# Kernel tuning notes

Measured on AMD Instinct MI355X. Metric: run time of the kernel, lower is better.

The kernel has to match this reference:

```python
import jax, jax.numpy as jnp
import numpy as np

H, F, L, T = 256, 128, 4, 1
NG, NC, EC, EG = 8192, 65536, 524288, 32768
NCONF, NMOL = 4096, 512
CUTOFF, NGAUSS = 10.0, 50
_OFF = jnp.linspace(0.0, CUTOFF, NGAUSS)
_COEFF = -0.5 / (_OFF[1] - _OFF[0]) ** 2


def _bn(h, g, b):
    # training-mode BatchNorm1d (biased variance, eps=1e-5)
    m = h.mean(0)
    v = h.var(0)
    return (h - m) * jax.lax.rsqrt(v + 1e-5) * g + b


def setup_inputs() -> dict:
    ks = iter(jax.random.split(jax.random.key(0), 64))
    nrm = lambda sh, s=0.05: jax.random.normal(next(ks), sh, jnp.float32) * s
    inp = dict(
        pos=jax.random.normal(next(ks), (NC, 3), jnp.float32) * 3.0,
        atom_emb=nrm((9, 64, H)),
        vn_emb=jnp.zeros((H,), jnp.float32),
        cf_lin1=nrm((L, H, F)),
        cf_mlp_w1=nrm((L, NGAUSS, F)), cf_mlp_b1=jnp.zeros((L, F)),
        cf_mlp_w2=nrm((L, F, F)), cf_mlp_b2=jnp.zeros((L, F)),
        cf_lin2=nrm((L, F, H)), cf_lin2_b=jnp.zeros((L, H)),
        lin_w=nrm((L, H, H)), lin_b=jnp.zeros((L, H)),
        bond_emb=nrm((L, 3, 8, H)), gin_eps=jnp.zeros((L,)),
        gin_w1=nrm((L, H, H)), gin_b1=jnp.zeros((L, H)),
        gin_g1=jnp.ones((L, H)), gin_be1=jnp.zeros((L, H)),
        gin_w2=nrm((L, H, H)), gin_b2=jnp.zeros((L, H)),
        bn_g=jnp.ones((L, H)), bn_b=jnp.zeros((L, H)),
        vn_w1=nrm((H, H)), vn_b1=jnp.zeros((H,)),
        vn_w2=nrm((H, H)), vn_b2=jnp.zeros((H,)),
        out_w1=nrm((H, H)), out_b1=jnp.zeros((H,)),
        out_w2=nrm((H, T)), out_b2=jnp.zeros((T,)),
    )
    inp['x_atom'] = jax.random.randint(next(ks), (NG, 9), 0, 64)
    g = np.arange(NG)
    reps = NC // NG  # 8 conformers per molecule
    inp['conf_node_batch'] = jnp.asarray(np.tile(g, reps))  # conformer node -> graph node
    mol = g // (NG // NMOL)  # 16 atoms per molecule
    inp['pos_batch'] = jnp.asarray(np.concatenate([mol * reps + r for r in range(reps)]))  # -> conformer id
    inp['conf_batch'] = jnp.asarray(np.arange(NCONF) // reps)  # conformer -> molecule
    inp['edge_index_conf'] = jax.random.randint(next(ks), (2, EC), 0, NC)
    inp['edge_index_graph'] = jax.random.randint(next(ks), (2, EG), 0, NG)
    inp['edge_attr_graph'] = jax.random.randint(next(ks), (EG, 3), 0, 8)
    return inp


def _forward(pos, atom_emb, vn_emb, cf_lin1, cf_mlp_w1, cf_mlp_b1, cf_mlp_w2, cf_mlp_b2,
             cf_lin2, cf_lin2_b, lin_w, lin_b, bond_emb, gin_eps, gin_w1, gin_b1,
             gin_g1, gin_be1, gin_w2, gin_b2, bn_g, bn_b, vn_w1, vn_b1, vn_w2, vn_b2,
             out_w1, out_b1, out_w2, out_b2,
             x_atom, conf_node_batch, pos_batch, conf_batch,
             edge_index_conf, edge_index_graph, edge_attr_graph):
    relu = jax.nn.relu
    # AtomEncoder: sum of per-feature embeddings [NG,H], broadcast to conformer nodes
    xg = atom_emb[jnp.arange(9), x_atom].sum(1)
    x = xg[conf_node_batch]                                 # [NC,H]
    # radius-graph geometry (edge list precomputed)
    src, dst = edge_index_conf[0], edge_index_conf[1]
    d = jnp.linalg.norm(pos[src] - pos[dst], axis=-1)       # [EC]
    gauss = jnp.exp(_COEFF * (d[:, None] - _OFF) ** 2)      # GaussianSmearing [EC,50]
    ccut = 0.5 * (jnp.cos(d * (jnp.pi / CUTOFF)) + 1.0)     # cosine cutoff
    gsrc, gdst = edge_index_graph[0], edge_index_graph[1]
    vn = jnp.broadcast_to(vn_emb, (NCONF, H))
    for i in range(L):
        x = x + vn[pos_batch]
        if i < L - 1:
            tmp = jax.ops.segment_sum(x, pos_batch, NCONF) + vn
            vn = relu(relu(tmp @ vn_w1 + vn_b1) @ vn_w2 + vn_b2)
        out = x  # residual
        # CFConv over conformer radius graph
        We = (relu(gauss @ cf_mlp_w1[i] + cf_mlp_b1[i]) @ cf_mlp_w2[i] + cf_mlp_b2[i]) * ccut[:, None]
        h = x @ cf_lin1[i]                                  # lin1 (no bias)
        h = jax.ops.segment_sum(h[src] * We, dst, NC)
        h = relu(h @ cf_lin2[i] + cf_lin2_b[i])
        out = out + h @ lin_w[i] + lin_b[i]
        # GIN over molecular graph on conf-max-pooled nodes
        xa = jax.ops.segment_max(x, conf_node_batch, NG)
        e = bond_emb[i][jnp.arange(3), edge_attr_graph].sum(1)   # BondEncoder [EG,H]
        agg = jax.ops.segment_sum(relu(xa[gsrc] + e), gdst, NG)
        z = ((1.0 + gin_eps[i]) * xa + agg) @ gin_w1[i] + gin_b1[i]
        z = relu(_bn(z, gin_g1[i], gin_be1[i])) @ gin_w2[i] + gin_b2[i]
        z = _bn(z, bn_g[i], bn_b[i])
        out = out + z[conf_node_batch]
        x = relu(out)
    xc = jax.ops.segment_max(x, pos_batch, NCONF)
    xm = jax.ops.segment_max(xc, conf_batch, NMOL)
    return relu(xm @ out_w1 + out_b1) @ out_w2 + out_b2      # [NMOL,T]


reference = _forward
```

## Files before the change

### kernel.cpp

```cpp
#include <hip/hip_runtime.h>
#include <math.h>

#define H 256
#define F 128
#define NLAYERS 4
#define NG 8192
#define NC 65536
#define EC 524288
#define EG 32768
#define NCONF 4096
#define NMOL 512
#define NGAUSS 50
#define NTAB 8192
#define TABSTEP 0.001953125f
#define INVSTEP 512.0f

using s16x8 = __attribute__((ext_vector_type(8))) short;
using f32x4 = __attribute__((ext_vector_type(4))) float;

static __device__ __forceinline__ unsigned short f2bf(float f) {
    unsigned int u = __float_as_uint(f);
    u += 0x7fffu + ((u >> 16) & 1u);
    return (unsigned short)(u >> 16);
}
static __device__ __forceinline__ float bf2f(unsigned short b) {
    return __uint_as_float(((unsigned int)b) << 16);
}
static __device__ __forceinline__ float bflo(unsigned int u) {
    return __uint_as_float(u << 16);
}
static __device__ __forceinline__ float bfhi(unsigned int u) {
    return __uint_as_float(u & 0xffff0000u);
}


__global__ __launch_bounds__(256) void k_init_x(const float* __restrict__ atom_emb,
    const int* __restrict__ x_atom, unsigned short* __restrict__ x)
{
    int i = blockIdx.x, h = threadIdx.x;
    int g = i & (NG - 1);
    float s = 0.f;
#pragma unroll
    for (int f = 0; f < 9; ++f) {
        int a = x_atom[g * 9 + f];
        s += atom_emb[(f * 64 + a) * H + h];
    }
    x[(size_t)i * H + h] = f2bf(s);
}

__global__ __launch_bounds__(256) void k_vninit(const float* __restrict__ vn_emb,
                                                float* __restrict__ vn)
{
    vn[(size_t)blockIdx.x * H + threadIdx.x] = vn_emb[threadIdx.x];
}

template <bool DOTMP>
__global__ __launch_bounds__(256) void k_pre(unsigned short* __restrict__ X,
    const float* __restrict__ vn, float* __restrict__ tmp,
    unsigned short* __restrict__ xa)
{
    int m = blockIdx.x, h = threadIdx.x;
    float xam[16];
#pragma unroll
    for (int t = 0; t < 16; ++t) xam[t] = -3.4e38f;
#pragma unroll 2
    for (int r = 0; r < 8; ++r) {
        float vv = vn[(size_t)(m * 8 + r) * H + h];
        float ts = vv;
        size_t base = ((size_t)r * NG + m * 16) * H + h;
#pragma unroll
        for (int t = 0; t < 16; ++t) {
            float v = bf2f(X[base + (size_t)t * H]) + vv;
            X[base + (size_t)t * H] = f2bf(v);
            xam[t] = fmaxf(xam[t], v);
            ts += v;
        }
        if (DOTMP) tmp[(size_t)(m * 8 + r) * H + h] = ts;
    }
#pragma unroll
    for (int t = 0; t < 16; ++t)
        xa[(size_t)(m * 16 + t) * H + h] = f2bf(xam[t]);
}

__global__ __launch_bounds__(256) void k_bnprep(const float* __restrict__ stats,
    const float* __restrict__ gamma, const float* __restrict__ beta,
    float* __restrict__ scale, float* __restrict__ shift)
{
    int n = threadIdx.x;
    float mean = stats[n] * (1.0f / NG);
    float var = stats[256 + n] * (1.0f / NG) - mean * mean;
    float sc = gamma[n] * rsqrtf(var + 1e-5f);
    scale[n] = sc;
    shift[n] = beta[n] - mean * sc;
}

__global__ __launch_bounds__(256) void k_molmax(const unsigned short* __restrict__ x,
                                                float* __restrict__ xm)
{
    int m = blockIdx.x, h = threadIdx.x;
    float best = -3.4e38f;
    for (int r = 0; r < 8; ++r) {
        size_t base = ((size_t)r * NG + m * 16) * H + h;
#pragma unroll 4
        for (int t = 0; t < 16; ++t) best = fmaxf(best, bf2f(x[base + (size_t)t * H]));
    }
    xm[(size_t)m * H + h] = best;
}

__global__ __launch_bounds__(256) void k_head(const float* __restrict__ y1,
    const float* __restrict__ w2, const float* __restrict__ b2,
    float* __restrict__ out)
{
    __shared__ float red[256];
    int m = blockIdx.x, h = threadIdx.x;
    red[h] = y1[(size_t)m * H + h] * w2[h];
    __syncthreads();
    for (int s = 128; s > 0; s >>= 1) {
        if (h < s) red[h] += red[h + s];
        __syncthreads();
    }
    if (h == 0) out[m] = red[0] + b2[0];
}

__global__ __launch_bounds__(256) void k_wt(const float* __restrict__ W,
    unsigned short* __restrict__ Wt, int K, int N, int Kp)
{
    int l = blockIdx.y;
    W += (size_t)l * K * N;
    Wt += (size_t)l * N * Kp;
    int n = blockIdx.x;
    for (int k = threadIdx.x; k < Kp; k += 256)
        Wt[(size_t)n * Kp + k] = (k < K) ? f2bf(W[(size_t)k * N + n]) : (unsigned short)0;
}


__global__ __launch_bounds__(256) void k_hist(const int* __restrict__ dst,
                                              int* __restrict__ cnt, int ne)
{
    int e = blockIdx.x * 256 + threadIdx.x;
    if (e < ne) atomicAdd(&cnt[dst[e]], 1);
}

__global__ __launch_bounds__(256) void k_scan1(const int* __restrict__ cnt,
    int* __restrict__ part, int* __restrict__ bsum)
{
    __shared__ int sh[256];
    int t = threadIdx.x, idx = blockIdx.x * 256 + t;
    int v = cnt[idx];
    sh[t] = v; __syncthreads();
    for (int s = 1; s < 256; s <<= 1) {
        int add = (t >= s) ? sh[t - s] : 0;
        __syncthreads();
        sh[t] += add;
        __syncthreads();
    }
    part[idx] = sh[t] - v;
    if (t == 255) bsum[blockIdx.x] = sh[255];
}

__global__ __launch_bounds__(256) void k_scan2(int* __restrict__ bsum, int nb)
{
    __shared__ int sh[256];
    int t = threadIdx.x;
    int v = (t < nb) ? bsum[t] : 0;
    sh[t] = v; __syncthreads();
    for (int s = 1; s < 256; s <<= 1) {
        int add = (t >= s) ? sh[t - s] : 0;
        __syncthreads();
        sh[t] += add;
        __syncthreads();
    }
    if (t < nb) bsum[t] = sh[t] - v;
}

__global__ __launch_bounds__(256) void k_scan3(int* __restrict__ part,
    const int* __restrict__ bsum, int* __restrict__ cursor, int nbins, int total)
{
    int idx = blockIdx.x * 256 + threadIdx.x;
    int v = part[idx] + bsum[blockIdx.x];
    part[idx] = v;
    cursor[idx] = v;
    if (idx == 0) part[nbins] = total;
}

__global__ __launch_bounds__(256) void k_cperm(const float* __restrict__ pos,
    const int* __restrict__ ei, int* __restrict__ cursor,
    int* __restrict__ psrc, float2* __restrict__ pdcc)
{
    int e = blockIdx.x * 256 + threadIdx.x;
    int s = ei[e], t = ei[EC + e];
    float dx = pos[s * 3 + 0] - pos[t * 3 + 0];
    float dy = pos[s * 3 + 1] - pos[t * 3 + 1];
    float dz = pos[s * 3 + 2] - pos[t * 3 + 2];
    float dd = sqrtf(dx * dx + dy * dy + dz * dz);
    int p = atomicAdd(&cursor[t], 1);
    psrc[p] = s;
    pdcc[p] = make_float2(dd, 0.5f * (cosf(dd * 0.314159265358979f) + 1.0f));
}

__global__ __launch_bounds__(256) void k_gperm(const int* __restrict__ ei,
    const int* __restrict__ attr, int* __restrict__ cursor,
    int* __restrict__ pgsrc, int* __restrict__ pattr)
{
    int e = blockIdx.x * 256 + threadIdx.x;
    int s = ei[e], t = ei[EG + e];
    int p = atomicAdd(&cursor[t], 1);
    pgsrc[p] = s;
    pattr[p] = attr[e * 3] | (attr[e * 3 + 1] << 4) | (attr[e * 3 + 2] << 8);
}


__global__ __launch_bounds__(256) void k_cf_agg(const unsigned short* __restrict__ tab,
    const int* __restrict__ rowptr, const int* __restrict__ psrc,
    const float2* __restrict__ pdcc,
    const unsigned short* __restrict__ cfh, unsigned short* __restrict__ hagg)
{
    int slot = threadIdx.x >> 4;
    int c8 = (threadIdx.x & 15) << 3;
    int n = blockIdx.x * 16 + slot;
    int lo = rowptr[n], hi = rowptr[n + 1];
    float a[8] = {0.f, 0.f, 0.f, 0.f, 0.f, 0.f, 0.f, 0.f};
    for (int e = lo; e < hi; ++e) {
        int s = psrc[e];
        float2 dc = pdcc[e];
        float u = dc.x * INVSTEP + 0.5f;
        int it = (int)u;
        if (it > NTAB - 1) it = NTAB - 1;
        uint4 T = *(const uint4*)&tab[(size_t)it * F + c8];
        uint4 HV = *(const uint4*)&cfh[(size_t)s * F + c8];
        float cc = dc.y;
        a[0] = fmaf(bflo(T.x) * cc, bflo(HV.x), a[0]);
        a[1] = fmaf(bfhi(T.x) * cc, bfhi(HV.x), a[1]);
        a[2] = fmaf(bflo(T.y) * cc, bflo(HV.y), a[2]);
        a[3] = fmaf(bfhi(T.y) * cc, bfhi(HV.y), a[3]);
        a[4] = fmaf(bflo(T.z) * cc, bflo(HV.z), a[4]);
        a[5] = fmaf(bfhi(T.z) * cc, bfhi(HV.z), a[5]);
        a[6] = fmaf(bflo(T.w) * cc, bflo(HV.w), a[6]);
        a[7] = fmaf(bfhi(T.w) * cc, bfhi(HV.w), a[7]);
    }
    uint4 o;
    o.x = ((unsigned)f2bf(a[1]) << 16) | f2bf(a[0]);
    o.y = ((unsigned)f2bf(a[3]) << 16) | f2bf(a[2]);
    o.z = ((unsigned)f2bf(a[5]) << 16) | f2bf(a[4]);
    o.w = ((unsigned)f2bf(a[7]) << 16) | f2bf(a[6]);
    *(uint4*)&hagg[(size_t)n * F + c8] = o;
}

__global__ __launch_bounds__(256) void k_gin_agg(const unsigned short* __restrict__ xa,
    const float* __restrict__ bond, const int* __restrict__ growptr,
    const int* __restrict__ pgsrc, const int* __restrict__ pattr,
    const float* __restrict__ eps_p, unsigned short* __restrict__ agg)
{
    int g = blockIdx.x, h = threadIdx.x;
    int lo = growptr[g], hi = growptr[g + 1];
    float acc = 0.f;
    for (int e = lo; e < hi; ++e) {
        int s = pgsrc[e], a = pattr[e];
        float v = bf2f(xa[(size_t)s * H + h])
                + bond[(a & 15) * H + h]
                + bond[(8 + ((a >> 4) & 15)) * H + h]
                + bond[(16 + (a >> 8)) * H + h];
        acc += fmaxf(v, 0.f);
    }
    agg[(size_t)g * H + h] =
        f2bf((1.0f + eps_p[0]) * bf2f(xa[(size_t)g * H + h]) + acc);
}

template<int ASRC, int EPI>
__global__ __launch_bounds__(256) void mgemm(
    const float* __restrict__ Af, const unsigned short* __restrict__ Ab,
    const unsigned short* __restrict__ Bt,
    const float* __restrict__ bias,
    float* __restrict__ Cf, unsigned short* __restrict__ Cb,
    int K, int Kp, int ldc,
    const float* __restrict__ sca, const float* __restrict__ sha,
    float* __restrict__ stats_out)
{
    __shared__ unsigned short As[128][72];
    __shared__ unsigned short Bs[128][72];
    const int tid = threadIdx.x;
    const int bm = blockIdx.y * 128;
    const int bn = blockIdx.x * 128;
    const int lane = tid & 63;
    const int wid = tid >> 6;
    const int wm = wid >> 1, wn = wid & 1;
    const int rsel = lane & 15, ksel = (lane >> 4) * 8;

    f32x4 acc[4][4];
#pragma unroll
    for (int a = 0; a < 4; ++a)
#pragma unroll
        for (int b = 0; b < 4; ++b) acc[a][b] = (f32x4){0.f, 0.f, 0.f, 0.f};

    for (int k0 = 0; k0 < Kp; k0 += 64) {
#pragma unroll
        for (int i = 0; i < 4; ++i) {
            int c = tid + i * 256;
            int row = c >> 3, kc = (c & 7) * 8;
            *(uint4*)&Bs[row][kc] =
                *(const uint4*)&Bt[(size_t)(bn + row) * Kp + k0 + kc];
        }
        if constexpr (ASRC == 0 || ASRC == 4) {
#pragma unroll
            for (int i = 0; i < 8; ++i) {
                int c = tid + i * 256;
                int row = c >> 4, kc = (c & 15) * 4;
                float4 v = *(const float4*)&Af[(size_t)(bm + row) * K + k0 + kc];
                if constexpr (ASRC == 4) {
                    float4 s4 = *(const float4*)&sca[k0 + kc];
                    float4 h4 = *(const float4*)&sha[k0 + kc];
                    v.x = fmaxf(fmaf(v.x, s4.x, h4.x), 0.f);
                    v.y = fmaxf(fmaf(v.y, s4.y, h4.y), 0.f);
                    v.z = fmaxf(fmaf(v.z, s4.z, h4.z), 0.f);
                    v.w = fmaxf(fmaf(v.w, s4.w, h4.w), 0.f);
                }
                ushort4 b;
                b.x = f2bf(v.x); b.y = f2bf(v.y); b.z = f2bf(v.z); b.w = f2bf(v.w);
                *(ushort4*)&As[row][kc] = b;
            }
        } else {
#pragma unroll
            for (int i = 0; i < 4; ++i) {
                int c = tid + i * 256;
                int row = c >> 3, kc = (c & 7) * 8;
                *(uint4*)&As[row][kc] =
                    *(const uint4*)&Ab[(size_t)(bm + row) * K + k0 + kc];
            }
        }
        __syncthreads();
#pragma unroll
        for (int kk = 0; kk < 64; kk += 32) {
            s16x8 af[4], bf[4];
#pragma unroll
            for (int mi = 0; mi < 4; ++mi)
                af[mi] = *(const s16x8*)&As[wm * 64 + mi * 16 + rsel][kk + ksel];
#pragma unroll
            for (int ni = 0; ni < 4; ++ni)
                bf[ni] = *(const s16x8*)&Bs[wn * 64 + ni * 16 + rsel][kk + ksel];
#pragma unroll
            for (int mi = 0; mi < 4; ++mi)
#pragma unroll
                for (int ni = 0; ni < 4; ++ni)
                    acc[mi][ni] = __builtin_amdgcn_mfma_f32_16x16x32_bf16(
                        af[mi], bf[ni], acc[mi][ni], 0, 0, 0);
        }
        __syncthreads();
    }

    float colS[4] = {0.f, 0.f, 0.f, 0.f};
    float colQ[4] = {0.f, 0.f, 0.f, 0.f};
#pragma unroll
    for (int mi = 0; mi < 4; ++mi) {
// ... 129 lines not shown
        __syncthreads();
#pragma unroll
        for (int kk = 0; kk < 64; kk += 32) {
            s16x8 af[4], bf[4];
#pragma unroll
            for (int mi = 0; mi < 4; ++mi)
                af[mi] = *(const s16x8*)&T1s[wm * 64 + mi * 16 + rsel][k0 + kk + ksel];
#pragma unroll
            for (int ni = 0; ni < 4; ++ni)
                bf[ni] = *(const s16x8*)&Bs[wn * 64 + ni * 16 + rsel][kk + ksel];
#pragma unroll
            for (int mi = 0; mi < 4; ++mi)
#pragma unroll
                for (int ni = 0; ni < 4; ++ni)
                    acc[mi][ni] = __builtin_amdgcn_mfma_f32_16x16x32_bf16(
                        af[mi], bf[ni], acc[mi][ni], 0, 0, 0);
        }
        __syncthreads();
    }
#pragma unroll
    for (int mi = 0; mi < 4; ++mi)
#pragma unroll
        for (int r = 0; r < 4; ++r) {
            int m = bm + wm * 64 + mi * 16 + ((lane >> 4) << 2) + r;
#pragma unroll
            for (int ni = 0; ni < 4; ++ni) {
                int n = wn * 64 + ni * 16 + (lane & 15);
                tab[(size_t)m * F + n] = f2bf(acc[mi][ni][r] + b2[n]);
            }
        }
}

__global__ __launch_bounds__(512) void k_vnmlp(
    const float* __restrict__ TMP,
    const unsigned short* __restrict__ w1, const float* __restrict__ b1,
    const unsigned short* __restrict__ w2, const float* __restrict__ b2,
    float* __restrict__ VN)
{
    __shared__ unsigned short As[128][72];
    __shared__ unsigned short Bs[256][72];
    __shared__ unsigned short Ts[128][264];
    const int tid = threadIdx.x;
    const int bm = blockIdx.x * 128;
    const int lane = tid & 63, wid = tid >> 6;
    const int wm = wid >> 2, wn = wid & 3;
    const int rsel = lane & 15, ksel = (lane >> 4) * 8;

    f32x4 acc[4][4];
#pragma unroll
    for (int a = 0; a < 4; ++a)
#pragma unroll
        for (int b = 0; b < 4; ++b) acc[a][b] = (f32x4){0.f, 0.f, 0.f, 0.f};
    for (int k0 = 0; k0 < 256; k0 += 64) {
#pragma unroll
        for (int i = 0; i < 4; ++i) {
            int c = tid + i * 512;
            int row = c >> 4, kc = (c & 15) * 4;
            float4 v = *(const float4*)&TMP[(size_t)(bm + row) * 256 + k0 + kc];
            ushort4 b;
            b.x = f2bf(v.x); b.y = f2bf(v.y); b.z = f2bf(v.z); b.w = f2bf(v.w);
            *(ushort4*)&As[row][kc] = b;
        }
#pragma unroll
        for (int i = 0; i < 4; ++i) {
            int c = tid + i * 512;
            int row = c >> 3, kc = (c & 7) * 8;
            *(uint4*)&Bs[row][kc] = *(const uint4*)&w1[(size_t)row * 256 + k0 + kc];
        }
        __syncthreads();
#pragma unroll
        for (int kk = 0; kk < 64; kk += 32) {
            s16x8 af[4], bf[4];
#pragma unroll
            for (int mi = 0; mi < 4; ++mi)
                af[mi] = *(const s16x8*)&As[wm * 64 + mi * 16 + rsel][kk + ksel];
#pragma unroll
            for (int ni = 0; ni < 4; ++ni)
                bf[ni] = *(const s16x8*)&Bs[wn * 64 + ni * 16 + rsel][kk + ksel];
#pragma unroll
            for (int mi = 0; mi < 4; ++mi)
#pragma unroll
                for (int ni = 0; ni < 4; ++ni)
                    acc[mi][ni] = __builtin_amdgcn_mfma_f32_16x16x32_bf16(
                        af[mi], bf[ni], acc[mi][ni], 0, 0, 0);
        }
        __syncthreads();
    }
#pragma unroll
    for (int mi = 0; mi < 4; ++mi)
#pragma unroll
        for (int r = 0; r < 4; ++r) {
            int mrow = wm * 64 + mi * 16 + ((lane >> 4) << 2) + r;
#pragma unroll
// ... 10 lines not shown
#pragma unroll
        for (int i = 0; i < 4; ++i) {
            int c = tid + i * 512;
            int row = c >> 3, kc = (c & 7) * 8;
            *(uint4*)&Bs[row][kc] = *(const uint4*)&w2[(size_t)row * 256 + k0 + kc];
        }
        __syncthreads();
#pragma unroll
        for (int kk = 0; kk < 64; kk += 32) {
            s16x8 af[4], bf[4];
#pragma unroll
            for (int mi = 0; mi < 4; ++mi)
                af[mi] = *(const s16x8*)&Ts[wm * 64 + mi * 16 + rsel][k0 + kk + ksel];
#pragma unroll
            for (int ni = 0; ni < 4; ++ni)
                bf[ni] = *(const s16x8*)&Bs[wn * 64 + ni * 16 + rsel][kk + ksel];
#pragma unroll
            for (int mi = 0; mi < 4; ++mi)
#pragma unroll
                for (int ni = 0; ni < 4; ++ni)
                    acc[mi][ni] = __builtin_amdgcn_mfma_f32_16x16x32_bf16(
                        af[mi], bf[ni], acc[mi][ni], 0, 0, 0);
        }
        __syncthreads();
    }
#pragma unroll
    for (int mi = 0; mi < 4; ++mi)
#pragma unroll
        for (int r = 0; r < 4; ++r) {
            int m = bm + wm * 64 + mi * 16 + ((lane >> 4) << 2) + r;
#pragma unroll
            for (int ni = 0; ni < 4; ++ni) {
                int n = wn * 64 + ni * 16 + (lane & 15);
                VN[(size_t)m * 256 + n] = fmaxf(acc[mi][ni][r] + b2[n], 0.f);
            }
        }
}

__global__ __launch_bounds__(512) void k_combine(
    const unsigned short* __restrict__ HAGG,
    const unsigned short* __restrict__ lin2t, const float* __restrict__ lin2b,
    const unsigned short* __restrict__ linwt, const float* __restrict__ linb,
    const float* __restrict__ Z2,
    const float* __restrict__ scb, const float* __restrict__ shb,
    unsigned short* __restrict__ X)
{
    __shared__ unsigned short As[128][72];
    __shared__ unsigned short Bs[256][72];
    __shared__ unsigned short H2s[128][264];
    const int tid = threadIdx.x;
    const int bm = blockIdx.x * 128;
    const int lane = tid & 63;
    const int wid = tid >> 6;
    const int wm = wid >> 2, wn = wid & 3;
    const int rsel = lane & 15, ksel = (lane >> 4) * 8;

    f32x4 acc[4][4];
#pragma unroll
    for (int a = 0; a < 4; ++a)
#pragma unroll
        for (int b = 0; b < 4; ++b) acc[a][b] = (f32x4){0.f, 0.f, 0.f, 0.f};

    for (int k0 = 0; k0 < 128; k0 += 64) {
#pragma unroll
        for (int i = 0; i < 2; ++i) {
            int c = tid + i * 512;
            int row = c >> 3, kc = (c & 7) * 8;
            *(uint4*)&As[row][kc] =
                *(const uint4*)&HAGG[(size_t)(bm + row) * 128 + k0 + kc];
        }
#pragma unroll
        for (int i = 0; i < 4; ++i) {
            int c = tid + i * 512;
            int row = c >> 3, kc = (c & 7) * 8;
            *(uint4*)&Bs[row][kc] = *(const uint4*)&lin2t[(size_t)row * 128 + k0 + kc];
        }
        __syncthreads();
#pragma unroll
// ... 27 lines not shown
        }

#pragma unroll
    for (int a = 0; a < 4; ++a)
#pragma unroll
        for (int b = 0; b < 4; ++b) acc[a][b] = (f32x4){0.f, 0.f, 0.f, 0.f};
    for (int k0 = 0; k0 < 256; k0 += 64) {
#pragma unroll
        for (int i = 0; i < 4; ++i) {
            int c = tid + i * 512;
            int row = c >> 3, kc = (c & 7) * 8;
            *(uint4*)&Bs[row][kc] = *(const uint4*)&linwt[(size_t)row * 256 + k0 + kc];
        }
        __syncthreads();
#pragma unroll
        for (int kk = 0; kk < 64; kk += 32) {
            s16x8 af[4], bf[4];
#pragma unroll
            for (int mi = 0; mi < 4; ++mi)
                af[mi] = *(const s16x8*)&H2s[wm * 64 + mi * 16 + rsel][k0 + kk + ksel];
#pragma unroll
            for (int ni = 0; ni < 4; ++ni)
                bf[ni] = *(const s16x8*)&Bs[wn * 64 + ni * 16 + rsel][kk + ksel];
#pragma unroll
            for (int mi = 0; mi < 4; ++mi)
#pragma unroll
                for (int ni = 0; ni < 4; ++ni)
                    acc[mi][ni] = __builtin_amdgcn_mfma_f32_16x16x32_bf16(
                        af[mi], bf[ni], acc[mi][ni], 0, 0, 0);
        }
        __syncthreads();
    }
#pragma unroll
    for (int mi = 0; mi < 4; ++mi)
#pragma unroll
        for (int r = 0; r < 4; ++r) {
            int m = bm + wm * 64 + mi * 16 + ((lane >> 4) << 2) + r;
            const float* z2row = &Z2[(size_t)(m & (NG - 1)) * 256];
#pragma unroll
            for (int ni = 0; ni < 4; ++ni) {
                int n = wn * 64 + ni * 16 + (lane & 15);
                size_t ix = (size_t)m * 256 + n;
                float z2v = fmaf(z2row[n], scb[n], shb[n]);
                float o = bf2f(X[ix]) + acc[mi][ni][r] + linb[n] + z2v;
                X[ix] = f2bf(fmaxf(o, 0.f));
            }
        }
}

extern "C" void kernel_launch(void* const* d_in, const int* in_sizes, int n_in,
                              void* d_out, int out_size, void* d_ws, size_t ws_size,
                              hipStream_t stream)
{
    (void)in_sizes; (void)n_in; (void)out_size; (void)ws_size;
    const float* pos       = (const float*)d_in[0];
    const float* atom_emb  = (const float*)d_in[1];
    const float* vn_emb    = (const float*)d_in[2];
    const float* cf_lin1   = (const float*)d_in[3];
    const float* cf_mlp_w1 = (const float*)d_in[4];
    const float* cf_mlp_b1 = (const float*)d_in[5];
    const float* cf_mlp_w2 = (const float*)d_in[6];
    const float* cf_mlp_b2 = (const float*)d_in[7];
    const float* cf_lin2   = (const float*)d_in[8];
    const float* cf_lin2_b = (const float*)d_in[9];
    const float* lin_w     = (const float*)d_in[10];
    const float* lin_b     = (const float*)d_in[11];
    const float* bond_emb  = (const float*)d_in[12];
    const float* gin_eps   = (const float*)d_in[13];
    const float* gin_w1    = (const float*)d_in[14];
    const float* gin_b1    = (const float*)d_in[15];
    const float* gin_g1    = (const float*)d_in[16];
    const float* gin_be1   = (const float*)d_in[17];
    const float* gin_w2    = (const float*)d_in[18];
    const float* gin_b2    = (const float*)d_in[19];
    const float* bn_g      = (const float*)d_in[20];
    const float* bn_b      = (const float*)d_in[21];
    const float* vn_w1     = (const float*)d_in[22];
    const float* vn_b1     = (const float*)d_in[23];
    const float* vn_w2     = (const float*)d_in[24];
    const float* vn_b2     = (const float*)d_in[25];
    const float* out_w1    = (const float*)d_in[26];
    const float* out_b1    = (const float*)d_in[27];
    const float* out_w2    = (const float*)d_in[28];
    const float* out_b2    = (const float*)d_in[29];
    const int* x_atom      = (const int*)d_in[30];
    const int* ei_conf     = (const int*)d_in[34];
    const int* ei_graph    = (const int*)d_in[35];
    const int* attr_graph  = (const int*)d_in[36];
    float* out = (float*)d_out;
    float* ws  = (float*)d_ws;

    size_t o = 0;
    float* Z1   = ws + o; o += (size_t)NG * H;
    float* Z2   = ws + o; o += (size_t)NG * H;
    float* VN   = ws + o; o += (size_t)NCONF * H;
    float* TMP  = ws + o; o += (size_t)NCONF * H;
    float* XM   = ws + o; o += (size_t)NMOL * H;
    float* Y1   = ws + o; o += (size_t)NMOL * H;
    float* STATS= ws + o; o += 1024;
    float* SCA  = ws + o; o += 256;
    float* SHA  = ws + o; o += 256;
    float* SCB  = ws + o; o += 256;
    float* SHB  = ws + o; o += 256;
    float* PDCC = ws + o; o += (size_t)2 * EC;
    unsigned short* XB   = (unsigned short*)(ws + o); o += (size_t)NC * H / 2;
    unsigned short* XA   = (unsigned short*)(ws + o); o += (size_t)NG * H / 2;
    unsigned short* AGGB = (unsigned short*)(ws + o); o += (size_t)NG * H / 2;
    unsigned short* CFH  = (unsigned short*)(ws + o); o += (size_t)NC * F / 2;
    unsigned short* HAGG = (unsigned short*)(ws + o); o += (size_t)NC * F / 2;
    unsigned short* TAB  = (unsigned short*)(ws + o); o += (size_t)NLAYERS * NTAB * F / 2;
    int* PSRC   = (int*)(ws + o); o += EC;
    int* PGSRC  = (int*)(ws + o); o += EG;
    int* PATTR  = (int*)(ws + o); o += EG;
    int* CNT    = (int*)(ws + o); o += NC;
    int* ROWC   = (int*)(ws + o); o += NC + 64;
    int* CURC   = (int*)(ws + o); o += NC;
    int* ROWG   = (int*)(ws + o); o += NG + 64;
    int* CURG   = (int*)(ws + o); o += NG;
    int* BSUM   = (int*)(ws + o); o += 256;
    unsigned short* WT = (unsigned short*)(ws + o);
    size_t wo = 0;
    unsigned short* lin1t = WT + wo; wo += (size_t)NLAYERS * 128 * 256;
    unsigned short* w1t   = WT + wo; wo += (size_t)NLAYERS * 128 * 64;
    unsigned short* w2t   = WT + wo; wo += (size_t)NLAYERS * 128 * 128;
    unsigned short* lin2t = WT + wo; wo += (size_t)NLAYERS * 256 * 128;
    unsigned short* linwt = WT + wo; wo += (size_t)NLAYERS * 256 * 256;
    unsigned short* g1t   = WT + wo; wo += (size_t)NLAYERS * 256 * 256;
    unsigned short* g2t   = WT + wo; wo += (size_t)NLAYERS * 256 * 256;
    unsigned short* vn1t  = WT + wo; wo += 256 * 256;
    unsigned short* vn2t  = WT + wo; wo += 256 * 256;
    unsigned short* ow1t  = WT + wo; wo += 256 * 256;

    k_wt<<<dim3(128, NLAYERS), 256, 0, stream>>>(cf_lin1,   lin1t, 256, 128, 256);
    k_wt<<<dim3(128, NLAYERS), 256, 0, stream>>>(cf_mlp_w1, w1t,    50, 128,  64);
    k_wt<<<dim3(128, NLAYERS), 256, 0, stream>>>(cf_mlp_w2, w2t,   128, 128, 128);
    k_wt<<<dim3(256, NLAYERS), 256, 0, stream>>>(cf_lin2,   lin2t, 128, 256, 128);
    k_wt<<<dim3(256, NLAYERS), 256, 0, stream>>>(lin_w,     linwt, 256, 256, 256);
    k_wt<<<dim3(256, NLAYERS), 256, 0, stream>>>(gin_w1,    g1t,   256, 256, 256);
    k_wt<<<dim3(256, NLAYERS), 256, 0, stream>>>(gin_w2,    g2t,   256, 256, 256);
    k_wt<<<dim3(256, 1), 256, 0, stream>>>(vn_w1,  vn1t, 256, 256, 256);
    k_wt<<<dim3(256, 1), 256, 0, stream>>>(vn_w2,  vn2t, 256, 256, 256);
    k_wt<<<dim3(256, 1), 256, 0, stream>>>(out_w1, ow1t, 256, 256, 256);
    k_tab<<<dim3(NTAB / 128, NLAYERS), 256, 0, stream>>>(
        w1t, cf_mlp_b1, w2t, cf_mlp_b2, TAB);

    hipMemsetAsync(CNT, 0, NC * sizeof(int), stream);
    k_hist<<<EC / 256, 256, 0, stream>>>(ei_conf + EC, CNT, EC);
    k_scan1<<<NC / 256, 256, 0, stream>>>(CNT, ROWC, BSUM);
    k_scan2<<<1, 256, 0, stream>>>(BSUM, NC / 256);
    k_scan3<<<NC / 256, 256, 0, stream>>>(ROWC, BSUM, CURC, NC, EC);
    k_cperm<<<EC / 256, 256, 0, stream>>>(pos, ei_conf, CURC, PSRC, (float2*)PDCC);

    hipMemsetAsync(CNT, 0, NG * sizeof(int), stream);
    k_hist<<<EG / 256, 256, 0, stream>>>(ei_graph + EG, CNT, EG);
    k_scan1<<<NG / 256, 256, 0, stream>>>(CNT, ROWG, BSUM);
    k_scan2<<<1, 256, 0, stream>>>(BSUM, NG / 256);
    k_scan3<<<NG / 256, 256, 0, stream>>>(ROWG, BSUM, CURG, NG, EG);
    k_gperm<<<EG / 256, 256, 0, stream>>>(ei_graph, attr_graph, CURG, PGSRC, PATTR);

    k_init_x<<<NC, 256, 0, stream>>>(atom_emb, x_atom, XB);
    k_vninit<<<NCONF, 256, 0, stream>>>(vn_emb, VN);

    for (int i = 0; i < NLAYERS; ++i) {
        if (i < NLAYERS - 1) {
            k_pre<true><<<NMOL, 256, 0, stream>>>(XB, VN, TMP, XA);
            k_vnmlp<<<NCONF / 128, 512, 0, stream>>>(TMP, vn1t, vn_b1, vn2t, vn_b2, VN);
        } else {
            k_pre<false><<<NMOL, 256, 0, stream>>>(XB, VN, TMP, XA);
        }
        mgemm<2, 6><<<dim3(1, NC / 128), 256, 0, stream>>>(
            0, XB, lin1t + (size_t)i * 128 * 256, nullptr, 0, CFH,
            256, 256, 128, 0, 0, 0);
        k_cf_agg<<<NC / 16, 256, 0, stream>>>(TAB + (size_t)i * NTAB * F,
            ROWC, PSRC, (const float2*)PDCC, CFH, HAGG);
        k_gin_agg<<<NG, 256, 0, stream>>>(
            XA, bond_emb + (size_t)i * 3 * 8 * H, ROWG, PGSRC, PATTR,
            gin_eps + i, AGGB);
        hipMemsetAsync(STATS, 0, 4096, stream);
        mgemm<2, 7><<<dim3(2, NG / 128), 256, 0, stream>>>(
            0, AGGB, g1t + (size_t)i * 256 * 256, gin_b1 + i * H, Z1, 0,
            256, 256, 256, 0, 0, STATS);
        k_bnprep<<<1, 256, 0, stream>>>(STATS, gin_g1 + i * H, gin_be1 + i * H,
                                        SCA, SHA);
        mgemm<4, 7><<<dim3(2, NG / 128), 256, 0, stream>>>(
            Z1, 0, g2t + (size_t)i * 256 * 256, gin_b2 + i * H, Z2, 0,
            256, 256, 256, SCA, SHA, STATS + 512);
        k_bnprep<<<1, 256, 0, stream>>>(STATS + 512, bn_g + i * H, bn_b + i * H,
                                        SCB, SHB);
        k_combine<<<NC / 128, 512, 0, stream>>>(
            HAGG, lin2t + (size_t)i * 256 * 128, cf_lin2_b + i * H,
            linwt + (size_t)i * 256 * 256, lin_b + i * H, Z2, SCB, SHB, XB);
    }

    k_molmax<<<NMOL, 256, 0, stream>>>(XB, XM);
    mgemm<0, 1><<<dim3(2, NMOL / 128), 256, 0, stream>>>(
        XM, 0, ow1t, out_b1, Y1, 0, 256, 256, 256, 0, 0, 0);
    k_head<<<NMOL, 256, 0, stream>>>(Y1, out_w2, out_b2, out);
}
```

Baseline: 984.9 us.

## Fold virtual-node add into consumers and fuse setup kernels

```diff
diff --git a/kernel.cpp b/kernel.cpp
--- a/kernel.cpp
+++ b/kernel.cpp
@@ -32,32 +32,35 @@
 static __device__ __forceinline__ float bfhi(unsigned int u) {
     return __uint_as_float(u & 0xffff0000u);
 }
-
+static __device__ __forceinline__ int conf_of(int i) {
+    return (((i & (NG - 1)) >> 4) << 3) + (i >> 13);
+}
 
 __global__ __launch_bounds__(256) void k_init_x(const float* __restrict__ atom_emb,
-    const int* __restrict__ x_atom, unsigned short* __restrict__ x)
-{
-    int i = blockIdx.x, h = threadIdx.x;
-    int g = i & (NG - 1);
-    float s = 0.f;
-#pragma unroll
-    for (int f = 0; f < 9; ++f) {
-        int a = x_atom[g * 9 + f];
-        s += atom_emb[(f * 64 + a) * H + h];
-    }
-    x[(size_t)i * H + h] = f2bf(s);
-}
-
-__global__ __launch_bounds__(256) void k_vninit(const float* __restrict__ vn_emb,
-                                                float* __restrict__ vn)
-{
-    vn[(size_t)blockIdx.x * H + threadIdx.x] = vn_emb[threadIdx.x];
-}
-
-template <bool DOTMP>
-__global__ __launch_bounds__(256) void k_pre(unsigned short* __restrict__ X,
-    const float* __restrict__ vn, float* __restrict__ tmp,
-    unsigned short* __restrict__ xa)
+    const int* __restrict__ x_atom, const float* __restrict__ vn_emb,
+    unsigned short* __restrict__ x, float* __restrict__ sumx,
+    float* __restrict__ vn0)
+{
+    int c = blockIdx.x, h = threadIdx.x;
+    int m = c >> 3, r = c & 7;
+    float sum = 0.f;
+    for (int t = 0; t < 16; ++t) {
+        int g = m * 16 + t;
+        float s = 0.f;
+#pragma unroll
+        for (int f = 0; f < 9; ++f) {
+            int a = x_atom[g * 9 + f];
+            s += atom_emb[(f * 64 + a) * H + h];
+        }
+        x[((size_t)r * NG + g) * H + h] = f2bf(s);
+        sum += s;
+    }
+    sumx[(size_t)c * H + h] = sum;
+    vn0[(size_t)c * H + h] = vn_emb[h];
+}
+
+__global__ __launch_bounds__(256) void k_xa2(const unsigned short* __restrict__ X,
+    const float* __restrict__ vn, unsigned short* __restrict__ xa)
 {
     int m = blockIdx.x, h = threadIdx.x;
     float xam[16];
@@ -66,16 +69,10 @@
 #pragma unroll 2
     for (int r = 0; r < 8; ++r) {
         float vv = vn[(size_t)(m * 8 + r) * H + h];
-        float ts = vv;
         size_t base = ((size_t)r * NG + m * 16) * H + h;
 #pragma unroll
-        for (int t = 0; t < 16; ++t) {
-            float v = bf2f(X[base + (size_t)t * H]) + vv;
-            X[base + (size_t)t * H] = f2bf(v);
-            xam[t] = fmaxf(xam[t], v);
-            ts += v;
-        }
-        if (DOTMP) tmp[(size_t)(m * 8 + r) * H + h] = ts;
+        for (int t = 0; t < 16; ++t)
+            xam[t] = fmaxf(xam[t], bf2f(X[base + (size_t)t * H]) + vv);
     }
 #pragma unroll
     for (int t = 0; t < 16; ++t)
@@ -122,31 +119,59 @@
     if (h == 0) out[m] = red[0] + b2[0];
 }
 
-__global__ __launch_bounds__(256) void k_wt(const float* __restrict__ W,
-    unsigned short* __restrict__ Wt, int K, int N, int Kp)
-{
-    int l = blockIdx.y;
-    W += (size_t)l * K * N;
+__global__ __launch_bounds__(256) void k_wprep(
+    const float* __restrict__ cf_lin1, const float* __restrict__ cf_mlp_w1,
+    const float* __restrict__ cf_mlp_w2, const float* __restrict__ cf_lin2,
+    const float* __restrict__ lin_w, const float* __restrict__ gin_w1,
+    const float* __restrict__ gin_w2, const float* __restrict__ vn_w1,
+    const float* __restrict__ vn_w2, const float* __restrict__ out_w1,
+    unsigned short* __restrict__ lin1t, unsigned short* __restrict__ w1t,
+    unsigned short* __restrict__ w2t, unsigned short* __restrict__ lin2t,
+    unsigned short* __restrict__ linwt, unsigned short* __restrict__ g1t,
+    unsigned short* __restrict__ g2t, unsigned short* __restrict__ vn1t,
+    unsigned short* __restrict__ vn2t, unsigned short* __restrict__ ow1t)
+{
+    int b = blockIdx.x;
+    const float* W; unsigned short* Wt; int K, N, Kp, l, n;
+    if (b < 512)      { b -= 0;    l = b >> 7; n = b & 127; W = cf_lin1;   Wt = lin1t; K = 256; N = 128; Kp = 256; }
+    else if (b < 1024){ b -= 512;  l = b >> 7; n = b & 127; W = cf_mlp_w1; Wt = w1t;   K = 50;  N = 128; Kp = 64;  }
+    else if (b < 1536){ b -= 1024; l = b >> 7; n = b & 127; W = cf_mlp_w2; Wt = w2t;   K = 128; N = 128; Kp = 128; }
+    else if (b < 2560){ b -= 1536; l = b >> 8; n = b & 255; W = cf_lin2;   Wt = lin2t; K = 128; N = 256; Kp = 128; }
+    else if (b < 3584){ b -= 2560; l = b >> 8; n = b & 255; W = lin_w;     Wt = linwt; K = 256; N = 256; Kp = 256; }
+    else if (b < 4608){ b -= 3584; l = b >> 8; n = b & 255; W = gin_w1;    Wt = g1t;   K = 256; N = 256; Kp = 256; }
+    else if (b < 5632){ b -= 4608; l = b >> 8; n = b & 255; W = gin_w2;    Wt = g2t;   K = 256; N = 256; Kp = 256; }
+    else if (b < 5888){ l = 0; n = b - 5632; W = vn_w1;  Wt = vn1t; K = 256; N = 256; Kp = 256; }
+    else if (b < 6144){ l = 0; n = b - 5888; W = vn_w2;  Wt = vn2t; K = 256; N = 256; Kp = 256; }
+    else              { l = 0; n = b - 6144; W = out_w1; Wt = ow1t; K = 256; N = 256; Kp = 256; }
+    W  += (size_t)l * K * N;
     Wt += (size_t)l * N * Kp;
-    int n = blockIdx.x;
     for (int k = threadIdx.x; k < Kp; k += 256)
         Wt[(size_t)n * Kp + k] = (k < K) ? f2bf(W[(size_t)k * N + n]) : (unsigned short)0;
 }
 
 
-__global__ __launch_bounds__(256) void k_hist(const int* __restrict__ dst,
-                                              int* __restrict__ cnt, int ne)
-{
-    int e = blockIdx.x * 256 + threadIdx.x;
-    if (e < ne) atomicAdd(&cnt[dst[e]], 1);
-}
-
-__global__ __launch_bounds__(256) void k_scan1(const int* __restrict__ cnt,
-    int* __restrict__ part, int* __restrict__ bsum)
+__global__ __launch_bounds__(256) void k_hist2(const int* __restrict__ ei_conf,
+    const int* __restrict__ ei_graph, int* __restrict__ cnt)
+{
+    int idx = blockIdx.x * 256 + threadIdx.x;
+    if (idx < EC) atomicAdd(&cnt[ei_conf[EC + idx]], 1);
+    else {
+        int j = idx - EC;
+        if (j < EG) atomicAdd(&cnt[NC + ei_graph[EG + j]], 1);
+    }
+}
+
+__global__ __launch_bounds__(256) void k_scan1m(const int* __restrict__ cnt,
+    int* __restrict__ rowc, int* __restrict__ rowg,
+    int* __restrict__ bsumc, int* __restrict__ bsumg)
 {
     __shared__ int sh[256];
-    int t = threadIdx.x, idx = blockIdx.x * 256 + t;
-    int v = cnt[idx];
+    int t = threadIdx.x, b = blockIdx.x;
+    const int* src; int* part; int* bsum; int bb;
+    if (b < 256) { src = cnt; part = rowc; bsum = bsumc; bb = b; }
+    else         { src = cnt + NC; part = rowg; bsum = bsumg; bb = b - 256; }
+    int idx = bb * 256 + t;
+    int v = src[idx];
     sh[t] = v; __syncthreads();
     for (int s = 1; s < 256; s <<= 1) {
         int add = (t >= s) ? sh[t - s] : 0;
@@ -155,14 +180,17 @@
         __syncthreads();
     }
     part[idx] = sh[t] - v;
-    if (t == 255) bsum[blockIdx.x] = sh[255];
-}
-
-__global__ __launch_bounds__(256) void k_scan2(int* __restrict__ bsum, int nb)
+    if (t == 255) bsum[bb] = sh[255];
+}
+
+__global__ __launch_bounds__(256) void k_scan2m(int* __restrict__ bsumc,
+                                                int* __restrict__ bsumg)
 {
     __shared__ int sh[256];
     int t = threadIdx.x;
-    int v = (t < nb) ? bsum[t] : 0;
+    int* bs = (blockIdx.x == 0) ? bsumc : bsumg;
+    int nb = (blockIdx.x == 0) ? 256 : 32;
+    int v = (t < nb) ? bs[t] : 0;
     sh[t] = v; __syncthreads();
     for (int s = 1; s < 256; s <<= 1) {
         int add = (t >= s) ? sh[t - s] : 0;
@@ -170,43 +198,53 @@
         sh[t] += add;
         __syncthreads();
     }
-    if (t < nb) bsum[t] = sh[t] - v;
-}
-
-__global__ __launch_bounds__(256) void k_scan3(int* __restrict__ part,
-    const int* __restrict__ bsum, int* __restrict__ cursor, int nbins, int total)
+    if (t < nb) bs[t] = sh[t] - v;
+}
+
+__global__ __launch_bounds__(256) void k_scan3m(int* __restrict__ rowc,
+    int* __restrict__ rowg, const int* __restrict__ bsumc,
+    const int* __restrict__ bsumg, int* __restrict__ curc, int* __restrict__ curg)
+{
+    int t = threadIdx.x, b = blockIdx.x;
+    if (b < 256) {
+        int idx = b * 256 + t;
+        int v = rowc[idx] + bsumc[b];
+        rowc[idx] = v; curc[idx] = v;
+        if (idx == 0) rowc[NC] = EC;
+    } else {
+        int bb = b - 256;
+        int idx = bb * 256 + t;
+        int v = rowg[idx] + bsumg[bb];
+        rowg[idx] = v; curg[idx] = v;
+        if (idx == 0) rowg[NG] = EG;
+    }
+}
+
+__global__ __launch_bounds__(256) void k_perm2(const float* __restrict__ pos,
+    const int* __restrict__ ei_conf, const int* __restrict__ ei_graph,
+    const int* __restrict__ attr, int* __restrict__ curc, int* __restrict__ curg,
+    int* __restrict__ psrc, float2* __restrict__ pdcc,
+    int* __restrict__ pgsrc, int* __restrict__ pattr)
 {
     int idx = blockIdx.x * 256 + threadIdx.x;
-    int v = part[idx] + bsum[blockIdx.x];
-    part[idx] = v;
-    cursor[idx] = v;
-    if (idx == 0) part[nbins] = total;
-}
-
-__global__ __launch_bounds__(256) void k_cperm(const float* __restrict__ pos,
-    const int* __restrict__ ei, int* __restrict__ cursor,
-    int* __restrict__ psrc, float2* __restrict__ pdcc)
-{
-    int e = blockIdx.x * 256 + threadIdx.x;
-    int s = ei[e], t = ei[EC + e];
-    float dx = pos[s * 3 + 0] - pos[t * 3 + 0];
-    float dy = pos[s * 3 + 1] - pos[t * 3 + 1];
-    float dz = pos[s * 3 + 2] - pos[t * 3 + 2];
-    float dd = sqrtf(dx * dx + dy * dy + dz * dz);
-    int p = atomicAdd(&cursor[t], 1);
-    psrc[p] = s;
-    pdcc[p] = make_float2(dd, 0.5f * (cosf(dd * 0.314159265358979f) + 1.0f));
-}
-
-__global__ __launch_bounds__(256) void k_gperm(const int* __restrict__ ei,
-    const int* __restrict__ attr, int* __restrict__ cursor,
-    int* __restrict__ pgsrc, int* __restrict__ pattr)
-{
-    int e = blockIdx.x * 256 + threadIdx.x;
-    int s = ei[e], t = ei[EG + e];
-    int p = atomicAdd(&cursor[t], 1);
-    pgsrc[p] = s;
-    pattr[p] = attr[e * 3] | (attr[e * 3 + 1] << 4) | (attr[e * 3 + 2] << 8);
+    if (idx < EC) {
+        int s = ei_conf[idx], t = ei_conf[EC + idx];
+        float dx = pos[s * 3 + 0] - pos[t * 3 + 0];
+        float dy = pos[s * 3 + 1] - pos[t * 3 + 1];
+        float dz = pos[s * 3 + 2] - pos[t * 3 + 2];
+        float dd = sqrtf(dx * dx + dy * dy + dz * dz);
+        int p = atomicAdd(&curc[t], 1);
+        psrc[p] = s;
+        pdcc[p] = make_float2(dd, 0.5f * (cosf(dd * 0.314159265358979f) + 1.0f));
+    } else {
+        int j = idx - EC;
+        if (j < EG) {
+            int s = ei_graph[j], t = ei_graph[EG + j];
+            int p = atomicAdd(&curg[t], 1);
+            pgsrc[p] = s;
+            pattr[p] = attr[j * 3] | (attr[j * 3 + 1] << 4) | (attr[j * 3 + 2] << 8);
+        }
+    }
 }
 
 
@@ -249,9 +287,14 @@
 __global__ __launch_bounds__(256) void k_gin_agg(const unsigned short* __restrict__ xa,
     const float* __restrict__ bond, const int* __restrict__ growptr,
     const int* __restrict__ pgsrc, const int* __restrict__ pattr,
-    const float* __restrict__ eps_p, unsigned short* __restrict__ agg)
+    const float* __restrict__ eps_p, unsigned short* __restrict__ agg,
+    float* __restrict__ stats)
 {
     int g = blockIdx.x, h = threadIdx.x;
+    if (g == 0) {
+#pragma unroll
+        for (int q = 0; q < 4; ++q) stats[q * 256 + h] = 0.f;
+    }
     int lo = growptr[g], hi = growptr[g + 1];
     float acc = 0.f;
     for (int e = lo; e < hi; ++e) {
@@ -274,7 +317,7 @@
     float* __restrict__ Cf, unsigned short* __restrict__ Cb,
     int K, int Kp, int ldc,
     const float* __restrict__ sca, const float* __restrict__ sha,
-    float* __restrict__ stats_out)
+    float* __restrict__ stats_out, const float* __restrict__ vnp)
 {
     __shared__ unsigned short As[128][72];
     __shared__ unsigned short Bs[128][72];
@@ -318,6 +361,24 @@
                 b.x = f2bf(v.x); b.y = f2bf(v.y); b.z = f2bf(v.z); b.w = f2bf(v.w);
                 *(ushort4*)&As[row][kc] = b;
             }
+        } else if constexpr (ASRC == 6) {
+#pragma unroll
+            for (int i = 0; i < 4; ++i) {
+                int c = tid + i * 256;
+                int row = c >> 3, kc = (c & 7) * 8;
+                int gm = bm + row;
+                int cf = conf_of(gm);
+                uint4 xv = *(const uint4*)&Ab[(size_t)gm * K + k0 + kc];
+                const float* vr = &vnp[(size_t)cf * 256 + k0 + kc];
+                float4 v0 = *(const float4*)vr;
+                float4 v1 = *(const float4*)(vr + 4);
+                uint4 o;
+                o.x = ((unsigned)f2bf(bfhi(xv.x) + v0.y) << 16) | f2bf(bflo(xv.x) + v0.x);
+                o.y = ((unsigned)f2bf(bfhi(xv.y) + v0.w) << 16) | f2bf(bflo(xv.y) + v0.z);
+                o.z = ((unsigned)f2bf(bfhi(xv.z) + v1.y) << 16) | f2bf(bflo(xv.z) + v1.x);
+                o.w = ((unsigned)f2bf(bfhi(xv.w) + v1.w) << 16) | f2bf(bflo(xv.w) + v1.z);
+                *(uint4*)&As[row][kc] = o;
+            }
         } else {
 #pragma unroll
             for (int i = 0; i < 4; ++i) {
@@ -513,10 +574,10 @@
 }
 
 __global__ __launch_bounds__(512) void k_vnmlp(
-    const float* __restrict__ TMP,
+    const float* __restrict__ SUMX, const float* __restrict__ VNin,
     const unsigned short* __restrict__ w1, const float* __restrict__ b1,
     const unsigned short* __restrict__ w2, const float* __restrict__ b2,
-    float* __restrict__ VN)
+    float* __restrict__ VNout)
 {
     __shared__ unsigned short As[128][72];
     __shared__ unsigned short Bs[256][72];
@@ -537,9 +598,14 @@
         for (int i = 0; i < 4; ++i) {
             int c = tid + i * 512;
             int row = c >> 4, kc = (c & 15) * 4;
-            float4 v = *(const float4*)&TMP[(size_t)(bm + row) * 256 + k0 + kc];
+            size_t off = (size_t)(bm + row) * 256 + k0 + kc;
+            float4 sx = *(const float4*)&SUMX[off];
+            float4 vv = *(const float4*)&VNin[off];
             ushort4 b;
-            b.x = f2bf(v.x); b.y = f2bf(v.y); b.z = f2bf(v.z); b.w = f2bf(v.w);
+            b.x = f2bf(fmaf(17.f, vv.x, sx.x));
+            b.y = f2bf(fmaf(17.f, vv.y, sx.y));
+            b.z = f2bf(fmaf(17.f, vv.z, sx.z));
+            b.w = f2bf(fmaf(17.f, vv.w, sx.w));
             *(ushort4*)&As[row][kc] = b;
         }
 #pragma unroll
@@ -616,18 +682,20 @@
 #pragma unroll
             for (int ni = 0; ni < 4; ++ni) {
                 int n = wn * 64 + ni * 16 + (lane & 15);
-                VN[(size_t)m * 256 + n] = fmaxf(acc[mi][ni][r] + b2[n], 0.f);
-            }
-        }
-}
-
+                VNout[(size_t)m * 256 + n] = fmaxf(acc[mi][ni][r] + b2[n], 0.f);
+            }
+        }
+}
+
+template <bool DOSUM>
 __global__ __launch_bounds__(512) void k_combine(
     const unsigned short* __restrict__ HAGG,
     const unsigned short* __restrict__ lin2t, const float* __restrict__ lin2b,
     const unsigned short* __restrict__ linwt, const float* __restrict__ linb,
     const float* __restrict__ Z2,
     const float* __restrict__ scb, const float* __restrict__ shb,
-    unsigned short* __restrict__ X)
+    const float* __restrict__ vn, unsigned short* __restrict__ X,
+    float* __restrict__ SUMX)
 {
     __shared__ unsigned short As[128][72];
     __shared__ unsigned short Bs[256][72];
@@ -721,20 +789,39 @@
         __syncthreads();
     }
 #pragma unroll
-    for (int mi = 0; mi < 4; ++mi)
+    for (int mi = 0; mi < 4; ++mi) {
+        int gm0 = bm + wm * 64 + mi * 16;
+        int cf = conf_of(gm0);
+        float srow[4] = {0.f, 0.f, 0.f, 0.f};
 #pragma unroll
         for (int r = 0; r < 4; ++r) {
-            int m = bm + wm * 64 + mi * 16 + ((lane >> 4) << 2) + r;
+            int m = gm0 + ((lane >> 4) << 2) + r;
             const float* z2row = &Z2[(size_t)(m & (NG - 1)) * 256];
 #pragma unroll
             for (int ni = 0; ni < 4; ++ni) {
                 int n = wn * 64 + ni * 16 + (lane & 15);
                 size_t ix = (size_t)m * 256 + n;
                 float z2v = fmaf(z2row[n], scb[n], shb[n]);
-                float o = bf2f(X[ix]) + acc[mi][ni][r] + linb[n] + z2v;
-                X[ix] = f2bf(fmaxf(o, 0.f));
-            }
-        }
+                float vnv = vn[(size_t)cf * 256 + n];
+                float o = bf2f(X[ix]) + vnv + acc[mi][ni][r] + linb[n] + z2v;
+                o = fmaxf(o, 0.f);
+                X[ix] = f2bf(o);
+                if (DOSUM) srow[ni] += o;
+            }
+        }
+        if (DOSUM) {
+#pragma unroll
+            for (int ni = 0; ni < 4; ++ni) {
+                float s = srow[ni];
+                s += __shfl_xor(s, 16);
+                s += __shfl_xor(s, 32);
+                if ((lane >> 4) == 0) {
+                    int n = wn * 64 + ni * 16 + (lane & 15);
+                    SUMX[(size_t)cf * 256 + n] = s;
+                }
+            }
+        }
+    }
 }
 
 extern "C" void kernel_launch(void* const* d_in, const int* in_sizes, int n_in,
@@ -782,8 +869,9 @@
     size_t o = 0;
     float* Z1   = ws + o; o += (size_t)NG * H;
     float* Z2   = ws + o; o += (size_t)NG * H;
-    float* VN   = ws + o; o += (size_t)NCONF * H;
-    float* TMP  = ws + o; o += (size_t)NCONF * H;
+    float* VN0  = ws + o; o += (size_t)NCONF * H;
+    float* VN1  = ws + o; o += (size_t)NCONF * H;
+    float* SUMX = ws + o; o += (size_t)NCONF * H;
     float* XM   = ws + o; o += (size_t)NMOL * H;
     float* Y1   = ws + o; o += (size_t)NMOL * H;
     float* STATS= ws + o; o += 1024;
@@ -801,12 +889,13 @@
     int* PSRC   = (int*)(ws + o); o += EC;
     int* PGSRC  = (int*)(ws + o); o += EG;
     int* PATTR  = (int*)(ws + o); o += EG;
-    int* CNT    = (int*)(ws + o); o += NC;
+    int* CNT    = (int*)(ws + o); o += NC + NG;
     int* ROWC   = (int*)(ws + o); o += NC + 64;
     int* CURC   = (int*)(ws + o); o += NC;
     int* ROWG   = (int*)(ws + o); o += NG + 64;
     int* CURG   = (int*)(ws + o); o += NG;
-    int* BSUM   = (int*)(ws + o); o += 256;
+    int* BSUMC  = (int*)(ws + o); o += 256;
+    int* BSUMG  = (int*)(ws + o); o += 64;
     unsigned short* WT = (unsigned short*)(ws + o);
     size_t wo = 0;
     unsigned short* lin1t = WT + wo; wo += (size_t)NLAYERS * 128 * 256;
@@ -820,69 +909,64 @@
     unsigned short* vn2t  = WT + wo; wo += 256 * 256;
     unsigned short* ow1t  = WT + wo; wo += 256 * 256;
 
-    k_wt<<<dim3(128, NLAYERS), 256, 0, stream>>>(cf_lin1,   lin1t, 256, 128, 256);
-    k_wt<<<dim3(128, NLAYERS), 256, 0, stream>>>(cf_mlp_w1, w1t,    50, 128,  64);
-    k_wt<<<dim3(128, NLAYERS), 256, 0, stream>>>(cf_mlp_w2, w2t,   128, 128, 128);
-    k_wt<<<dim3(256, NLAYERS), 256, 0, stream>>>(cf_lin2,   lin2t, 128, 256, 128);
-    k_wt<<<dim3(256, NLAYERS), 256, 0, stream>>>(lin_w,     linwt, 256, 256, 256);
-    k_wt<<<dim3(256, NLAYERS), 256, 0, stream>>>(gin_w1,    g1t,   256, 256, 256);
-    k_wt<<<dim3(256, NLAYERS), 256, 0, stream>>>(gin_w2,    g2t,   256, 256, 256);
-    k_wt<<<dim3(256, 1), 256, 0, stream>>>(vn_w1,  vn1t, 256, 256, 256);
-    k_wt<<<dim3(256, 1), 256, 0, stream>>>(vn_w2,  vn2t, 256, 256, 256);
-    k_wt<<<dim3(256, 1), 256, 0, stream>>>(out_w1, ow1t, 256, 256, 256);
+    k_wprep<<<6400, 256, 0, stream>>>(
+        cf_lin1, cf_mlp_w1, cf_mlp_w2, cf_lin2, lin_w, gin_w1, gin_w2,
+        vn_w1, vn_w2, out_w1,
+        lin1t, w1t, w2t, lin2t, linwt, g1t, g2t, vn1t, vn2t, ow1t);
     k_tab<<<dim3(NTAB / 128, NLAYERS), 256, 0, stream>>>(
         w1t, cf_mlp_b1, w2t, cf_mlp_b2, TAB);
 
-    hipMemsetAsync(CNT, 0, NC * sizeof(int), stream);
-    k_hist<<<EC / 256, 256, 0, stream>>>(ei_conf + EC, CNT, EC);
-    k_scan1<<<NC / 256, 256, 0, stream>>>(CNT, ROWC, BSUM);
-    k_scan2<<<1, 256, 0, stream>>>(BSUM, NC / 256);
-    k_scan3<<<NC / 256, 256, 0, stream>>>(ROWC, BSUM, CURC, NC, EC);
-    k_cperm<<<EC / 256, 256, 0, stream>>>(pos, ei_conf, CURC, PSRC, (float2*)PDCC);
-
-    hipMemsetAsync(CNT, 0, NG * sizeof(int), stream);
-    k_hist<<<EG / 256, 256, 0, stream>>>(ei_graph + EG, CNT, EG);
-    k_scan1<<<NG / 256, 256, 0, stream>>>(CNT, ROWG, BSUM);
-    k_scan2<<<1, 256, 0, stream>>>(BSUM, NG / 256);
-    k_scan3<<<NG / 256, 256, 0, stream>>>(ROWG, BSUM, CURG, NG, EG);
-    k_gperm<<<EG / 256, 256, 0, stream>>>(ei_graph, attr_graph, CURG, PGSRC, PATTR);
-
-    k_init_x<<<NC, 256, 0, stream>>>(atom_emb, x_atom, XB);
-    k_vninit<<<NCONF, 256, 0, stream>>>(vn_emb, VN);
-
+    hipMemsetAsync(CNT, 0, (NC + NG) * sizeof(int), stream);
+    k_hist2<<<(EC + EG) / 256, 256, 0, stream>>>(ei_conf, ei_graph, CNT);
+    k_scan1m<<<288, 256, 0, stream>>>(CNT, ROWC, ROWG, BSUMC, BSUMG);
+    k_scan2m<<<2, 256, 0, stream>>>(BSUMC, BSUMG);
+    k_scan3m<<<288, 256, 0, stream>>>(ROWC, ROWG, BSUMC, BSUMG, CURC, CURG);
+    k_perm2<<<(EC + EG) / 256, 256, 0, stream>>>(
+        pos, ei_conf, ei_graph, attr_graph, CURC, CURG,
+        PSRC, (float2*)PDCC, PGSRC, PATTR);
+
+    k_init_x<<<NCONF, 256, 0, stream>>>(atom_emb, x_atom, vn_emb, XB, SUMX, VN0);
+
+    float* vc = VN0;
+    float* vx = VN1;
     for (int i = 0; i < NLAYERS; ++i) {
-        if (i < NLAYERS - 1) {
-            k_pre<true><<<NMOL, 256, 0, stream>>>(XB, VN, TMP, XA);
-            k_vnmlp<<<NCONF / 128, 512, 0, stream>>>(TMP, vn1t, vn_b1, vn2t, vn_b2, VN);
-        } else {
-            k_pre<false><<<NMOL, 256, 0, stream>>>(XB, VN, TMP, XA);
-        }
-        mgemm<2, 6><<<dim3(1, NC / 128), 256, 0, stream>>>(
+        if (i < NLAYERS - 1)
+            k_vnmlp<<<NCONF / 128, 512, 0, stream>>>(
+                SUMX, vc, vn1t, vn_b1, vn2t, vn_b2, vx);
+        mgemm<6, 6><<<dim3(1, NC / 128), 256, 0, stream>>>(
             0, XB, lin1t + (size_t)i * 128 * 256, nullptr, 0, CFH,
-            256, 256, 128, 0, 0, 0);
+            256, 256, 128, 0, 0, 0, vc);
         k_cf_agg<<<NC / 16, 256, 0, stream>>>(TAB + (size_t)i * NTAB * F,
             ROWC, PSRC, (const float2*)PDCC, CFH, HAGG);
+        k_xa2<<<NMOL, 256, 0, stream>>>(XB, vc, XA);
         k_gin_agg<<<NG, 256, 0, stream>>>(
             XA, bond_emb + (size_t)i * 3 * 8 * H, ROWG, PGSRC, PATTR,
-            gin_eps + i, AGGB);
-        hipMemsetAsync(STATS, 0, 4096, stream);
+            gin_eps + i, AGGB, STATS);
         mgemm<2, 7><<<dim3(2, NG / 128), 256, 0, stream>>>(
             0, AGGB, g1t + (size_t)i * 256 * 256, gin_b1 + i * H, Z1, 0,
-            256, 256, 256, 0, 0, STATS);
+            256, 256, 256, 0, 0, STATS, 0);
         k_bnprep<<<1, 256, 0, stream>>>(STATS, gin_g1 + i * H, gin_be1 + i * H,
                                         SCA, SHA);
         mgemm<4, 7><<<dim3(2, NG / 128), 256, 0, stream>>>(
             Z1, 0, g2t + (size_t)i * 256 * 256, gin_b2 + i * H, Z2, 0,
-            256, 256, 256, SCA, SHA, STATS + 512);
+            256, 256, 256, SCA, SHA, STATS + 512, 0);
         k_bnprep<<<1, 256, 0, stream>>>(STATS + 512, bn_g + i * H, bn_b + i * H,
                                         SCB, SHB);
-        k_combine<<<NC / 128, 512, 0, stream>>>(
-            HAGG, lin2t + (size_t)i * 256 * 128, cf_lin2_b + i * H,
-            linwt + (size_t)i * 256 * 256, lin_b + i * H, Z2, SCB, SHB, XB);
+        if (i < NLAYERS - 1)
+            k_combine<true><<<NC / 128, 512, 0, stream>>>(
+                HAGG, lin2t + (size_t)i * 256 * 128, cf_lin2_b + i * H,
+                linwt + (size_t)i * 256 * 256, lin_b + i * H, Z2, SCB, SHB,
+                vc, XB, SUMX);
+        else
+            k_combine<false><<<NC / 128, 512, 0, stream>>>(
+                HAGG, lin2t + (size_t)i * 256 * 128, cf_lin2_b + i * H,
+                linwt + (size_t)i * 256 * 256, lin_b + i * H, Z2, SCB, SHB,
+                vc, XB, SUMX);
+        float* t = vc; vc = vx; vx = t;
     }
 
     k_molmax<<<NMOL, 256, 0, stream>>>(XB, XM);
     mgemm<0, 1><<<dim3(2, NMOL / 128), 256, 0, stream>>>(
-        XM, 0, ow1t, out_b1, Y1, 0, 256, 256, 256, 0, 0, 0);
+        XM, 0, ow1t, out_b1, Y1, 0, 256, 256, 256, 0, 0, 0, 0);
     k_head<<<NMOL, 256, 0, stream>>>(Y1, out_w2, out_b2, out);
 }
```

After: 946.6 us. -3.9%, faster.
